# Optimization experiments

Measured on AMD Instinct MI355X. Metric: run time of the kernel, lower is better.

## Reference

```python
import jax, jax.numpy as jnp
import numpy as np

B, N = 16384, 4096
PERCENT_ON = 0.1
TEMPERATURE = 10.0  # training-mode temperature
K = int(round(N * PERCENT_ON))  # 410


def setup_inputs() -> dict:
    key = jax.random.key(0)
    k1, k2 = jax.random.split(key)
    x = jax.random.normal(k1, (B, N), dtype=jnp.float32)
    # Gumbel noise for sampling-without-replacement (Gumbel-top-k trick),
    # equivalent to torch.multinomial(softmax(x/T), k, replacement=False).
    gumbel = jax.random.gumbel(k2, (B, N), dtype=jnp.float32)
    return {"x": x, "gumbel": gumbel}


def reference(x, gumbel):
    # logits with temperature
    logits = x / TEMPERATURE
    # entropy of the categorical distribution per row, averaged (single stable pass)
    logp = jax.nn.log_softmax(logits, axis=-1)
    entropy = jnp.mean(-jnp.sum(jnp.exp(logp) * logp, axis=-1))
    # sample K winners without replacement via Gumbel-top-k
    _, idx = jax.lax.top_k(logits + gumbel, K)  # idx: [B, K]
    rows = jnp.arange(x.shape[0])[:, None]       # [B, 1]
    mask = jnp.zeros_like(x).at[rows, idx].set(1.0)
    out = x * mask  # relu=False path
    return out, entropy
```

## Files before the change

### kernel.cpp

```cpp
#include <hip/hip_runtime.h>
#include <math.h>

#define TPB 256
#define EPT 16
#define NN  4096
#define KSEL 410
#define CAP 1024

typedef float floatx4 __attribute__((ext_vector_type(4)));

__device__ __forceinline__ unsigned sortkey(float f) {
    unsigned u = __float_as_uint(f);
    unsigned m = (unsigned)(((int)u) >> 31);
    return u ^ (m | 0x80000000u);
}

template <bool USE_WS>
__global__ __launch_bounds__(TPB)
void skw_main(const float* __restrict__ x, const float* __restrict__ g,
              float* __restrict__ out, float* __restrict__ rowH,
              float* __restrict__ entAcc, float invB)
{
    const int row  = blockIdx.x;
    const int t    = threadIdx.x;
    const int w    = t >> 6;
    const int lane = t & 63;
    const size_t rbase = (size_t)row * NN;

    float    xv[EPT];
    unsigned key[EPT];
    unsigned bp[EPT / 4];

    __shared__ unsigned hist0[256][9];
    __shared__ unsigned wtot[4];
    __shared__ unsigned wtA[4], wtB[4];
    __shared__ float    fred[8];
    __shared__ unsigned sh_digit, sh_above, sh_cnt, sh_thr, sh_take;

    unsigned* list = &hist0[0][0];

    const float4* xp = reinterpret_cast<const float4*>(x + rbase);
    const float4* gp = reinterpret_cast<const float4*>(g + rbase);
    floatx4*      op = reinterpret_cast<floatx4*>(out + rbase);

    float sZ = 0.f, sZL = 0.f;
#pragma unroll
    for (int q = 0; q < EPT / 4; ++q) {
        float4 xx = xp[(q << 8) + t];
        float4 gg = gp[(q << 8) + t];
        float xa[4] = {xx.x, xx.y, xx.z, xx.w};
        float ga[4] = {gg.x, gg.y, gg.z, gg.w};
        unsigned pk = 0;
#pragma unroll
        for (int jj = 0; jj < 4; ++jj) {
            float xs = xa[jj];
            xv[4 * q + jj] = xs;
            float l = xs * 0.1f;
            float e = __expf(l);
            sZ  += e;
            sZL = __builtin_fmaf(e, l, sZL);
            float q10 = __builtin_fmaf(__builtin_fmaf(-10.0f, l, xs), 0.1f, l);
            float s = q10 + ga[jj];
            key[4 * q + jj] = sortkey(s);
            int b = (int)__builtin_fmaf(s, 16.0f, 64.0f);
            b = min(max(b, 0), 255);
            pk |= (unsigned)b << (8 * jj);
        }
        bp[q] = pk;
    }

#pragma unroll
    for (int sft = 32; sft >= 1; sft >>= 1) { sZ += __shfl_xor(sZ, sft); sZL += __shfl_xor(sZL, sft); }
    if (lane == 0) { fred[w] = sZ; fred[4 + w] = sZL; }

    unsigned* h0 = &hist0[0][0];
#pragma unroll
    for (int i = 0; i < 9; ++i) h0[t + 256 * i] = 0;
    if (t == 0) sh_cnt = 0;
    __syncthreads();

    if (t == 0) {
        float Z = fred[0] + fred[1] + fred[2] + fred[3];
        float L = fred[4] + fred[5] + fred[6] + fred[7];
        float H = __logf(Z) - L / Z;
        if (USE_WS) rowH[row] = H;
        else atomicAdd(entAcc, H * invB);
    }

#pragma unroll
    for (int q = 0; q < EPT / 4; ++q) {
        unsigned pk = bp[q];
#pragma unroll
        for (int jj = 0; jj < 4; ++jj)
            atomicAdd(&hist0[(pk >> (8 * jj)) & 255u][lane & 7], 1u);
    }
    __syncthreads();

    unsigned v = 0;
#pragma unroll
    for (int k = 0; k < 8; ++k) v += hist0[t][k];
#pragma unroll
    for (int sft = 1; sft < 64; sft <<= 1) {
        unsigned tmp = __shfl(v, lane + sft);
        v += (lane + sft < 64) ? tmp : 0u;
    }
    if (lane == 0) wtot[w] = v;
    unsigned vnext = __shfl(v, lane + 1);
    __syncthreads();
    unsigned Kr = KSEL;
    {
        unsigned hi = 0;
#pragma unroll
        for (int c = 0; c < 4; ++c) hi += (c > w) ? wtot[c] : 0u;
        unsigned cum     = v + hi;
        unsigned cumNext = ((lane < 63) ? vnext : 0u) + hi;
        if (cum >= Kr && cumNext < Kr) { sh_digit = (unsigned)t; sh_above = cumNext; }
    }
    __syncthreads();
    const unsigned Bstar = sh_digit;
    Kr -= sh_above;

    unsigned cm = 0;
#pragma unroll
    for (int q = 0; q < EPT / 4; ++q) {
        unsigned pk = bp[q];
#pragma unroll
        for (int jj = 0; jj < 4; ++jj)
            cm |= (((pk >> (8 * jj)) & 255u) == Bstar) ? (1u << (4 * q + jj)) : 0u;
    }
#pragma unroll
    for (int j = 0; j < EPT; ++j) {
        if ((cm >> j) & 1u) {
            unsigned p = atomicAdd(&sh_cnt, 1u);
            if (p < CAP) list[p] = key[j];
        }
    }
    __syncthreads();

    const unsigned M = sh_cnt;
    for (unsigned i = t; i < M; i += TPB) {
        unsigned ki = list[i];
        unsigned gt = 0, eqc = 0;
        for (unsigned j2 = 0; j2 < M; ++j2) {
            unsigned kj = list[j2];
            gt  += (kj > ki) ? 1u : 0u;
            eqc += (kj == ki) ? 1u : 0u;
        }
        if (gt < Kr && Kr <= gt + eqc) { sh_thr = ki; sh_take = Kr - gt; }
    }
    __syncthreads();
    const unsigned thr    = sh_thr;
    const unsigned KrTake = sh_take;

    unsigned eq[4];
#pragma unroll
    for (int q = 0; q < 4; ++q) {
        unsigned e = 0;
#pragma unroll
        for (int jj = 0; jj < 4; ++jj) e += (key[4 * q + jj] == thr) ? 1u : 0u;
        eq[q] = e;
    }
    unsigned wA = eq[0] | (eq[1] << 16);
    unsigned wB = eq[2] | (eq[3] << 16);
    unsigned sA = wA, sB = wB;
#pragma unroll
    for (int sft = 1; sft < 64; sft <<= 1) {
        unsigned ta = __shfl(sA, lane - sft);
        unsigned tb = __shfl(sB, lane - sft);
        if (lane >= sft) { sA += ta; sB += tb; }
    }
    if (lane == 63) { wtA[w] = sA; wtB[w] = sB; }
    __syncthreads();
    unsigned offA = 0, offB = 0, totA = 0, totB = 0;
#pragma unroll
    for (int c = 0; c < 4; ++c) {
        totA += wtA[c]; totB += wtB[c];
        if (c < w) { offA += wtA[c]; offB += wtB[c]; }
    }
    unsigned exA = offA + sA - wA;
    unsigned exB = offB + sB - wB;
    unsigned tot0 = totA & 0xFFFFu, tot1 = totA >> 16, tot2 = totB & 0xFFFFu;
    unsigned baseq[4] = {0u, tot0, tot0 + tot1, tot0 + tot1 + tot2};
    unsigned exq[4]   = {exA & 0xFFFFu, exA >> 16, exB & 0xFFFFu, exB >> 16};

#pragma unroll
    for (int q = 0; q < EPT / 4; ++q) {
        unsigned pos = baseq[q] + exq[q];
        float vals[4];
#pragma unroll
        for (int jj = 0; jj < 4; ++jj) {
            int j = 4 * q + jj;
            bool sel;
            if (key[j] > thr)       sel = true;
            else if (key[j] == thr) { sel = (pos < KrTake); ++pos; }
            else                    sel = false;
            vals[jj] = sel ? xv[j] : 0.0f;
        }
        floatx4 o4;
        o4.x = vals[0]; o4.y = vals[1]; o4.z = vals[2]; o4.w = vals[3];
        __builtin_nontemporal_store(o4, &op[(q << 8) + t]);
    }
}

__global__ void skw_zero(float* p) { *p = 0.0f; }

__global__ void skw_reduce(const float* __restrict__ rowH, float* __restrict__ outp, int B)
{
    __shared__ float red[256];
    int t = threadIdx.x;
    float s = 0.f;
    for (int i = t; i < B; i += 256) s += rowH[i];
    red[t] = s; __syncthreads();
    for (int st = 128; st > 0; st >>= 1) { if (t < st) red[t] += red[t + st]; __syncthreads(); }
    if (t == 0) *outp = red[0] / (float)B;
}

extern "C" void kernel_launch(void* const* d_in, const int* in_sizes, int n_in,
                              void* d_out, int out_size, void* d_ws, size_t ws_size,
                              hipStream_t stream)
{
    const float* x = (const float*)d_in[0];
    const float* g = (const float*)d_in[1];
    float* out = (float*)d_out;
    const int BN = in_sizes[0];
    const int B  = BN / NN;
    float* entp = out + (size_t)BN;

    if (ws_size >= (size_t)B * sizeof(float)) {
        float* rowH = (float*)d_ws;
        skw_main<true><<<B, TPB, 0, stream>>>(x, g, out, rowH, nullptr, 0.f);
        skw_reduce<<<1, 256, 0, stream>>>(rowH, entp, B);
    } else {
        skw_zero<<<1, 1, 0, stream>>>(entp);
        skw_main<false><<<B, TPB, 0, stream>>>(x, g, out, nullptr, entp, 1.0f / (float)B);
    }
}
```

Before: 166.9 us.

## Use 1024 threads per row with one float4 per thread

Each row block now has 1024 threads, and each thread handles a single float4 of x and gumbel instead of four. This drops the per-thread arrays and the packed 16-bit two-lane prefix scan, and uses 16 waves for the reductions and the tie-break scan. Histogram scanning stays on the first 4 waves, and both branches still hit the barrier. The aim is lower register pressure and more loads in flight on a kernel limited by memory bandwidth. The cost is more barrier participants and a longer cross-wave reduction.

```diff
diff --git a/kernel.cpp b/kernel.cpp
--- a/kernel.cpp
+++ b/kernel.cpp
@@ -1,8 +1,9 @@
 #include <hip/hip_runtime.h>
 #include <math.h>
 
-#define TPB 256
-#define EPT 16
+#define TPB 1024
+#define EPT 4
+#define NW  16
 #define NN  4096
 #define KSEL 410
 #define CAP 1024
@@ -27,14 +28,12 @@
     const int lane = t & 63;
     const size_t rbase = (size_t)row * NN;
 
-    float    xv[EPT];
     unsigned key[EPT];
-    unsigned bp[EPT / 4];
 
     __shared__ unsigned hist0[256][9];
     __shared__ unsigned wtot[4];
-    __shared__ unsigned wtA[4], wtB[4];
-    __shared__ float    fred[8];
+    __shared__ unsigned wt16[NW];
+    __shared__ float    fred[2 * NW];
     __shared__ unsigned sh_digit, sh_above, sh_cnt, sh_thr, sh_take;
 
     unsigned* list = &hist0[0][0];
@@ -43,96 +42,81 @@
     const float4* gp = reinterpret_cast<const float4*>(g + rbase);
     floatx4*      op = reinterpret_cast<floatx4*>(out + rbase);
 
+    float4 xx = xp[t];
+    float4 gg = gp[t];
+
+    float xa[4] = {xx.x, xx.y, xx.z, xx.w};
+    float ga[4] = {gg.x, gg.y, gg.z, gg.w};
     float sZ = 0.f, sZL = 0.f;
-#pragma unroll
-    for (int q = 0; q < EPT / 4; ++q) {
-        float4 xx = xp[(q << 8) + t];
-        float4 gg = gp[(q << 8) + t];
-        float xa[4] = {xx.x, xx.y, xx.z, xx.w};
-        float ga[4] = {gg.x, gg.y, gg.z, gg.w};
-        unsigned pk = 0;
-#pragma unroll
-        for (int jj = 0; jj < 4; ++jj) {
-            float xs = xa[jj];
-            xv[4 * q + jj] = xs;
-            float l = xs * 0.1f;
-            float e = __expf(l);
-            sZ  += e;
-            sZL = __builtin_fmaf(e, l, sZL);
-            float q10 = __builtin_fmaf(__builtin_fmaf(-10.0f, l, xs), 0.1f, l);
-            float s = q10 + ga[jj];
-            key[4 * q + jj] = sortkey(s);
-            int b = (int)__builtin_fmaf(s, 16.0f, 64.0f);
-            b = min(max(b, 0), 255);
-            pk |= (unsigned)b << (8 * jj);
-        }
-        bp[q] = pk;
+    unsigned pk = 0;
+#pragma unroll
+    for (int jj = 0; jj < 4; ++jj) {
+        float xs = xa[jj];
+        float l = xs * 0.1f;
+        float e = __expf(l);
+        sZ  += e;
+        sZL = __builtin_fmaf(e, l, sZL);
+        float q10 = __builtin_fmaf(__builtin_fmaf(-10.0f, l, xs), 0.1f, l);
+        float s = q10 + ga[jj];
+        key[jj] = sortkey(s);
+        int b = (int)__builtin_fmaf(s, 16.0f, 64.0f);
+        b = min(max(b, 0), 255);
+        pk |= (unsigned)b << (8 * jj);
     }
 
 #pragma unroll
     for (int sft = 32; sft >= 1; sft >>= 1) { sZ += __shfl_xor(sZ, sft); sZL += __shfl_xor(sZL, sft); }
-    if (lane == 0) { fred[w] = sZ; fred[4 + w] = sZL; }
+    if (lane == 0) { fred[w] = sZ; fred[NW + w] = sZL; }
 
     unsigned* h0 = &hist0[0][0];
-#pragma unroll
-    for (int i = 0; i < 9; ++i) h0[t + 256 * i] = 0;
+    for (int i = t; i < 256 * 9; i += TPB) h0[i] = 0;
     if (t == 0) sh_cnt = 0;
     __syncthreads();
 
     if (t == 0) {
-        float Z = fred[0] + fred[1] + fred[2] + fred[3];
-        float L = fred[4] + fred[5] + fred[6] + fred[7];
+        float Z = 0.f, L = 0.f;
+#pragma unroll
+        for (int c = 0; c < NW; ++c) { Z += fred[c]; L += fred[NW + c]; }
         float H = __logf(Z) - L / Z;
         if (USE_WS) rowH[row] = H;
         else atomicAdd(entAcc, H * invB);
     }
 
 #pragma unroll
-    for (int q = 0; q < EPT / 4; ++q) {
-        unsigned pk = bp[q];
-#pragma unroll
-        for (int jj = 0; jj < 4; ++jj)
-            atomicAdd(&hist0[(pk >> (8 * jj)) & 255u][lane & 7], 1u);
-    }
-    __syncthreads();
-
-    unsigned v = 0;
-#pragma unroll
-    for (int k = 0; k < 8; ++k) v += hist0[t][k];
-#pragma unroll
-    for (int sft = 1; sft < 64; sft <<= 1) {
-        unsigned tmp = __shfl(v, lane + sft);
-        v += (lane + sft < 64) ? tmp : 0u;
-    }
-    if (lane == 0) wtot[w] = v;
-    unsigned vnext = __shfl(v, lane + 1);
-    __syncthreads();
-    unsigned Kr = KSEL;
-    {
+    for (int jj = 0; jj < 4; ++jj)
+        atomicAdd(&hist0[(pk >> (8 * jj)) & 255u][lane & 7], 1u);
+    __syncthreads();
+
+    if (t < 256) {
+        unsigned v = 0;
+#pragma unroll
+        for (int k = 0; k < 8; ++k) v += hist0[t][k];
+#pragma unroll
+        for (int sft = 1; sft < 64; sft <<= 1) {
+            unsigned tmp = __shfl(v, lane + sft);
+            v += (lane + sft < 64) ? tmp : 0u;
+        }
+        if (lane == 0) wtot[w] = v;
+        unsigned vnext = __shfl(v, lane + 1);
+        __syncthreads();
         unsigned hi = 0;
 #pragma unroll
         for (int c = 0; c < 4; ++c) hi += (c > w) ? wtot[c] : 0u;
         unsigned cum     = v + hi;
         unsigned cumNext = ((lane < 63) ? vnext : 0u) + hi;
-        if (cum >= Kr && cumNext < Kr) { sh_digit = (unsigned)t; sh_above = cumNext; }
+        if (cum >= KSEL && cumNext < KSEL) { sh_digit = (unsigned)t; sh_above = cumNext; }
+    } else {
+        __syncthreads();
     }
     __syncthreads();
     const unsigned Bstar = sh_digit;
-    Kr -= sh_above;
-
-    unsigned cm = 0;
-#pragma unroll
-    for (int q = 0; q < EPT / 4; ++q) {
-        unsigned pk = bp[q];
-#pragma unroll
-        for (int jj = 0; jj < 4; ++jj)
-            cm |= (((pk >> (8 * jj)) & 255u) == Bstar) ? (1u << (4 * q + jj)) : 0u;
-    }
-#pragma unroll
-    for (int j = 0; j < EPT; ++j) {
-        if ((cm >> j) & 1u) {
+    const unsigned Kr = KSEL - sh_above;
+
+#pragma unroll
+    for (int jj = 0; jj < 4; ++jj) {
+        if (((pk >> (8 * jj)) & 255u) == Bstar) {
             unsigned p = atomicAdd(&sh_cnt, 1u);
-            if (p < CAP) list[p] = key[j];
+            if (p < CAP) list[p] = key[jj];
         }
     }
     __syncthreads();
@@ -152,54 +136,34 @@
     const unsigned thr    = sh_thr;
     const unsigned KrTake = sh_take;
 
-    unsigned eq[4];
-#pragma unroll
-    for (int q = 0; q < 4; ++q) {
-        unsigned e = 0;
-#pragma unroll
-        for (int jj = 0; jj < 4; ++jj) e += (key[4 * q + jj] == thr) ? 1u : 0u;
-        eq[q] = e;
-    }
-    unsigned wA = eq[0] | (eq[1] << 16);
-    unsigned wB = eq[2] | (eq[3] << 16);
-    unsigned sA = wA, sB = wB;
+    unsigned eq = 0;
+#pragma unroll
+    for (int jj = 0; jj < 4; ++jj) eq += (key[jj] == thr) ? 1u : 0u;
+    unsigned sv = eq;
 #pragma unroll
     for (int sft = 1; sft < 64; sft <<= 1) {
-        unsigned ta = __shfl(sA, lane - sft);
-        unsigned tb = __shfl(sB, lane - sft);
-        if (lane >= sft) { sA += ta; sB += tb; }
-    }
-    if (lane == 63) { wtA[w] = sA; wtB[w] = sB; }
-    __syncthreads();
-    unsigned offA = 0, offB = 0, totA = 0, totB = 0;
-#pragma unroll
-    for (int c = 0; c < 4; ++c) {
-        totA += wtA[c]; totB += wtB[c];
-        if (c < w) { offA += wtA[c]; offB += wtB[c]; }
-    }
-    unsigned exA = offA + sA - wA;
-    unsigned exB = offB + sB - wB;
-    unsigned tot0 = totA & 0xFFFFu, tot1 = totA >> 16, tot2 = totB & 0xFFFFu;
-    unsigned baseq[4] = {0u, tot0, tot0 + tot1, tot0 + tot1 + tot2};
-    unsigned exq[4]   = {exA & 0xFFFFu, exA >> 16, exB & 0xFFFFu, exB >> 16};
-
-#pragma unroll
-    for (int q = 0; q < EPT / 4; ++q) {
-        unsigned pos = baseq[q] + exq[q];
-        float vals[4];
-#pragma unroll
-        for (int jj = 0; jj < 4; ++jj) {
-            int j = 4 * q + jj;
-            bool sel;
-            if (key[j] > thr)       sel = true;
-            else if (key[j] == thr) { sel = (pos < KrTake); ++pos; }
-            else                    sel = false;
-            vals[jj] = sel ? xv[j] : 0.0f;
-        }
-        floatx4 o4;
-        o4.x = vals[0]; o4.y = vals[1]; o4.z = vals[2]; o4.w = vals[3];
-        __builtin_nontemporal_store(o4, &op[(q << 8) + t]);
-    }
+        unsigned tmp = __shfl(sv, lane - sft);
+        sv += (lane >= sft) ? tmp : 0u;
+    }
+    if (lane == 63) wt16[w] = sv;
+    __syncthreads();
+    unsigned offset = 0;
+#pragma unroll
+    for (int c = 0; c < NW; ++c) offset += (c < w) ? wt16[c] : 0u;
+    unsigned pos = offset + sv - eq;
+
+    float vals[4];
+#pragma unroll
+    for (int jj = 0; jj < 4; ++jj) {
+        bool sel;
+        if (key[jj] > thr)       sel = true;
+        else if (key[jj] == thr) { sel = (pos < KrTake); ++pos; }
+        else                     sel = false;
+        vals[jj] = sel ? xa[jj] : 0.0f;
+    }
+    floatx4 o4;
+    o4.x = vals[0]; o4.y = vals[1]; o4.z = vals[2]; o4.w = vals[3];
+    __builtin_nontemporal_store(o4, &op[t]);
 }
 
 __global__ void skw_zero(float* p) { *p = 0.0f; }
```

Measured after the change: 227.2 us. 36.2% more time.

## Process eight rows per block with double-buffered async global-to-LDS prefetch

Applied to the files above, without the earlier changes.

Each block now handles eight consecutive rows instead of one. While the current row is processed from LDS, the x and gumbel data for the next row are loaded into a second LDS buffer with global_load_lds, so load latency overlaps the histogram and selection work. The intent is to hide HBM latency and cut per-block launch overhead. The cost is a 64 KB LDS staging buffer per block, which lowers how many blocks can be resident per CU. The hand-written vmcnt waits also depend on how the earlier non-temporal stores are counted, and a wrong count could let a row be read before its prefetch has landed.

```diff
diff --git a/kernel.cpp b/kernel.cpp
--- a/kernel.cpp
+++ b/kernel.cpp
@@ -6,6 +6,7 @@
 #define NN  4096
 #define KSEL 410
 #define CAP 1024
+#define ROWS 8
 
 typedef float floatx4 __attribute__((ext_vector_type(4)));
 
@@ -15,22 +16,45 @@
     return u ^ (m | 0x80000000u);
 }
 
+__device__ __forceinline__ void dma16(const float* gsrc, float* lds) {
+    __builtin_amdgcn_global_load_lds(
+        (__attribute__((address_space(1))) void*)(void*)gsrc,
+        (__attribute__((address_space(3))) void*)(void*)lds,
+        16, 0, 0);
+}
+
+__device__ __forceinline__ void barsync() {
+    asm volatile("s_waitcnt lgkmcnt(0)" ::: "memory");
+    __builtin_amdgcn_s_barrier();
+}
+
+#define VMWAIT(N) do { \
+    asm volatile("s_waitcnt vmcnt(" #N ")" ::: "memory"); \
+    __builtin_amdgcn_sched_barrier(0); \
+} while (0)
+
+#define ISSUE_DMA(rw, b) do { \
+    const float* xr_ = x + (size_t)(rw) * NN; \
+    const float* gr_ = g + (size_t)(rw) * NN; \
+    float* sb_ = &stage[b][w * 2048]; \
+    _Pragma("unroll") \
+    for (int q_ = 0; q_ < 4; ++q_) { \
+        dma16(xr_ + q_ * 1024 + w * 256 + lane * 4, sb_ + q_ * 256); \
+        dma16(gr_ + q_ * 1024 + w * 256 + lane * 4, sb_ + 1024 + q_ * 256); \
+    } \
+} while (0)
+
 template <bool USE_WS>
 __global__ __launch_bounds__(TPB)
 void skw_main(const float* __restrict__ x, const float* __restrict__ g,
               float* __restrict__ out, float* __restrict__ rowH,
-              float* __restrict__ entAcc, float invB)
+              float* __restrict__ entAcc, float invB, int nrows)
 {
-    const int row  = blockIdx.x;
     const int t    = threadIdx.x;
     const int w    = t >> 6;
     const int lane = t & 63;
-    const size_t rbase = (size_t)row * NN;
-
-    float    xv[EPT];
-    unsigned key[EPT];
-    unsigned bp[EPT / 4];
-
+
+    __shared__ float    stage[2][8192];
     __shared__ unsigned hist0[256][9];
     __shared__ unsigned wtot[4];
     __shared__ unsigned wtA[4], wtB[4];
@@ -39,166 +63,183 @@
 
     unsigned* list = &hist0[0][0];
 
-    const float4* xp = reinterpret_cast<const float4*>(x + rbase);
-    const float4* gp = reinterpret_cast<const float4*>(g + rbase);
-    floatx4*      op = reinterpret_cast<floatx4*>(out + rbase);
-
-    float sZ = 0.f, sZL = 0.f;
-#pragma unroll
-    for (int q = 0; q < EPT / 4; ++q) {
-        float4 xx = xp[(q << 8) + t];
-        float4 gg = gp[(q << 8) + t];
-        float xa[4] = {xx.x, xx.y, xx.z, xx.w};
-        float ga[4] = {gg.x, gg.y, gg.z, gg.w};
-        unsigned pk = 0;
-#pragma unroll
-        for (int jj = 0; jj < 4; ++jj) {
-            float xs = xa[jj];
-            xv[4 * q + jj] = xs;
-            float l = xs * 0.1f;
-            float e = __expf(l);
-            sZ  += e;
-            sZL = __builtin_fmaf(e, l, sZL);
-            float q10 = __builtin_fmaf(__builtin_fmaf(-10.0f, l, xs), 0.1f, l);
-            float s = q10 + ga[jj];
-            key[4 * q + jj] = sortkey(s);
-            int b = (int)__builtin_fmaf(s, 16.0f, 64.0f);
-            b = min(max(b, 0), 255);
-            pk |= (unsigned)b << (8 * jj);
-        }
-        bp[q] = pk;
-    }
-
-#pragma unroll
-    for (int sft = 32; sft >= 1; sft >>= 1) { sZ += __shfl_xor(sZ, sft); sZL += __shfl_xor(sZL, sft); }
-    if (lane == 0) { fred[w] = sZ; fred[4 + w] = sZL; }
-
-    unsigned* h0 = &hist0[0][0];
-#pragma unroll
-    for (int i = 0; i < 9; ++i) h0[t + 256 * i] = 0;
-    if (t == 0) sh_cnt = 0;
-    __syncthreads();
-
-    if (t == 0) {
-        float Z = fred[0] + fred[1] + fred[2] + fred[3];
-        float L = fred[4] + fred[5] + fred[6] + fred[7];
-        float H = __logf(Z) - L / Z;
-        if (USE_WS) rowH[row] = H;
-        else atomicAdd(entAcc, H * invB);
-    }
-
-#pragma unroll
-    for (int q = 0; q < EPT / 4; ++q) {
-        unsigned pk = bp[q];
-#pragma unroll
-        for (int jj = 0; jj < 4; ++jj)
-            atomicAdd(&hist0[(pk >> (8 * jj)) & 255u][lane & 7], 1u);
-    }
-    __syncthreads();
-
-    unsigned v = 0;
-#pragma unroll
-    for (int k = 0; k < 8; ++k) v += hist0[t][k];
-#pragma unroll
-    for (int sft = 1; sft < 64; sft <<= 1) {
-        unsigned tmp = __shfl(v, lane + sft);
-        v += (lane + sft < 64) ? tmp : 0u;
-    }
-    if (lane == 0) wtot[w] = v;
-    unsigned vnext = __shfl(v, lane + 1);
-    __syncthreads();
-    unsigned Kr = KSEL;
-    {
-        unsigned hi = 0;
-#pragma unroll
-        for (int c = 0; c < 4; ++c) hi += (c > w) ? wtot[c] : 0u;
-        unsigned cum     = v + hi;
-        unsigned cumNext = ((lane < 63) ? vnext : 0u) + hi;
-        if (cum >= Kr && cumNext < Kr) { sh_digit = (unsigned)t; sh_above = cumNext; }
-    }
-    __syncthreads();
-    const unsigned Bstar = sh_digit;
-    Kr -= sh_above;
-
-    unsigned cm = 0;
-#pragma unroll
-    for (int q = 0; q < EPT / 4; ++q) {
-        unsigned pk = bp[q];
-#pragma unroll
-        for (int jj = 0; jj < 4; ++jj)
-            cm |= (((pk >> (8 * jj)) & 255u) == Bstar) ? (1u << (4 * q + jj)) : 0u;
-    }
-#pragma unroll
-    for (int j = 0; j < EPT; ++j) {
-        if ((cm >> j) & 1u) {
-            unsigned p = atomicAdd(&sh_cnt, 1u);
-            if (p < CAP) list[p] = key[j];
-        }
-    }
-    __syncthreads();
-
-    const unsigned M = sh_cnt;
-    for (unsigned i = t; i < M; i += TPB) {
-        unsigned ki = list[i];
-        unsigned gt = 0, eqc = 0;
-        for (unsigned j2 = 0; j2 < M; ++j2) {
-            unsigned kj = list[j2];
-            gt  += (kj > ki) ? 1u : 0u;
-            eqc += (kj == ki) ? 1u : 0u;
-        }
-        if (gt < Kr && Kr <= gt + eqc) { sh_thr = ki; sh_take = Kr - gt; }
-    }
-    __syncthreads();
-    const unsigned thr    = sh_thr;
-    const unsigned KrTake = sh_take;
-
-    unsigned eq[4];
-#pragma unroll
-    for (int q = 0; q < 4; ++q) {
-        unsigned e = 0;
-#pragma unroll
-        for (int jj = 0; jj < 4; ++jj) e += (key[4 * q + jj] == thr) ? 1u : 0u;
-        eq[q] = e;
-    }
-    unsigned wA = eq[0] | (eq[1] << 16);
-    unsigned wB = eq[2] | (eq[3] << 16);
-    unsigned sA = wA, sB = wB;
-#pragma unroll
-    for (int sft = 1; sft < 64; sft <<= 1) {
-        unsigned ta = __shfl(sA, lane - sft);
-        unsigned tb = __shfl(sB, lane - sft);
-        if (lane >= sft) { sA += ta; sB += tb; }
-    }
-    if (lane == 63) { wtA[w] = sA; wtB[w] = sB; }
-    __syncthreads();
-    unsigned offA = 0, offB = 0, totA = 0, totB = 0;
-#pragma unroll
-    for (int c = 0; c < 4; ++c) {
-        totA += wtA[c]; totB += wtB[c];
-        if (c < w) { offA += wtA[c]; offB += wtB[c]; }
-    }
-    unsigned exA = offA + sA - wA;
-    unsigned exB = offB + sB - wB;
-    unsigned tot0 = totA & 0xFFFFu, tot1 = totA >> 16, tot2 = totB & 0xFFFFu;
-    unsigned baseq[4] = {0u, tot0, tot0 + tot1, tot0 + tot1 + tot2};
-    unsigned exq[4]   = {exA & 0xFFFFu, exA >> 16, exB & 0xFFFFu, exB >> 16};
-
-#pragma unroll
-    for (int q = 0; q < EPT / 4; ++q) {
-        unsigned pos = baseq[q] + exq[q];
-        float vals[4];
-#pragma unroll
-        for (int jj = 0; jj < 4; ++jj) {
-            int j = 4 * q + jj;
-            bool sel;
-            if (key[j] > thr)       sel = true;
-            else if (key[j] == thr) { sel = (pos < KrTake); ++pos; }
-            else                    sel = false;
-            vals[jj] = sel ? xv[j] : 0.0f;
-        }
-        floatx4 o4;
-        o4.x = vals[0]; o4.y = vals[1]; o4.z = vals[2]; o4.w = vals[3];
-        __builtin_nontemporal_store(o4, &op[(q << 8) + t]);
+    const int r0 = blockIdx.x * ROWS;
+    if (r0 >= nrows) return;
+    const int rend = (r0 + ROWS < nrows) ? (r0 + ROWS) : nrows;
+
+    int cur = 0;
+    ISSUE_DMA(r0, 0);
+
+#pragma unroll 1
+    for (int row = r0; row < rend; ++row) {
+        if (row == r0) { VMWAIT(0); } else { VMWAIT(8); }
+
+        if (row + 1 < rend) ISSUE_DMA(row + 1, cur ^ 1);
+
+        const float4* sx = reinterpret_cast<const float4*>(&stage[cur][w * 2048]);
+
+        float    xc[EPT];
+        unsigned key[EPT];
+        unsigned bp[EPT / 4];
+        float sZ = 0.f, sZL = 0.f;
+#pragma unroll
+        for (int q = 0; q < EPT / 4; ++q) {
+            float4 xx = sx[q * 64 + lane];
+            float4 gg = sx[256 + q * 64 + lane];
+            float xa[4] = {xx.x, xx.y, xx.z, xx.w};
+            float ga[4] = {gg.x, gg.y, gg.z, gg.w};
+            unsigned pk = 0;
+#pragma unroll
+            for (int jj = 0; jj < 4; ++jj) {
+                float xs = xa[jj];
+                xc[4 * q + jj] = xs;
+                float l = xs * 0.1f;
+                float e = __expf(l);
+                sZ  += e;
+                sZL = __builtin_fmaf(e, l, sZL);
+                float q10 = __builtin_fmaf(__builtin_fmaf(-10.0f, l, xs), 0.1f, l);
+                float s = q10 + ga[jj];
+                key[4 * q + jj] = sortkey(s);
+                int b = (int)__builtin_fmaf(s, 16.0f, 64.0f);
+                b = min(max(b, 0), 255);
+                pk |= (unsigned)b << (8 * jj);
+            }
+            bp[q] = pk;
+        }
+
+#pragma unroll
+        for (int sft = 32; sft >= 1; sft >>= 1) { sZ += __shfl_xor(sZ, sft); sZL += __shfl_xor(sZL, sft); }
+        if (lane == 0) { fred[w] = sZ; fred[4 + w] = sZL; }
+
+        unsigned* h0 = &hist0[0][0];
+#pragma unroll
+        for (int i = 0; i < 9; ++i) h0[t + 256 * i] = 0;
+        if (t == 0) sh_cnt = 0;
+        barsync();
+
+        if (t == 0) {
+            float Z = fred[0] + fred[1] + fred[2] + fred[3];
+            float L = fred[4] + fred[5] + fred[6] + fred[7];
+            float H = __logf(Z) - L / Z;
+            if (USE_WS) rowH[row] = H;
+            else atomicAdd(entAcc, H * invB);
+        }
+
+#pragma unroll
+        for (int q = 0; q < EPT / 4; ++q) {
+            unsigned pk = bp[q];
+#pragma unroll
+            for (int jj = 0; jj < 4; ++jj)
+                atomicAdd(&hist0[(pk >> (8 * jj)) & 255u][lane & 7], 1u);
+        }
+        barsync();
+
+        unsigned v = 0;
+#pragma unroll
+        for (int k = 0; k < 8; ++k) v += hist0[t][k];
+#pragma unroll
+        for (int sft = 1; sft < 64; sft <<= 1) {
+            unsigned tmp = __shfl(v, lane + sft);
+            v += (lane + sft < 64) ? tmp : 0u;
+        }
+        if (lane == 0) wtot[w] = v;
+        unsigned vnext = __shfl(v, lane + 1);
+        barsync();
+        unsigned Kr = KSEL;
+        {
+            unsigned hi = 0;
+#pragma unroll
+            for (int c = 0; c < 4; ++c) hi += (c > w) ? wtot[c] : 0u;
+            unsigned cum     = v + hi;
+            unsigned cumNext = ((lane < 63) ? vnext : 0u) + hi;
+            if (cum >= Kr && cumNext < Kr) { sh_digit = (unsigned)t; sh_above = cumNext; }
+        }
+        barsync();
+        const unsigned Bstar = sh_digit;
+        Kr -= sh_above;
+
+        unsigned cm = 0;
+#pragma unroll
+        for (int q = 0; q < EPT / 4; ++q) {
+            unsigned pk = bp[q];
+#pragma unroll
+            for (int jj = 0; jj < 4; ++jj)
+                cm |= (((pk >> (8 * jj)) & 255u) == Bstar) ? (1u << (4 * q + jj)) : 0u;
+        }
+#pragma unroll
+        for (int j = 0; j < EPT; ++j) {
+            if ((cm >> j) & 1u) {
+                unsigned p = atomicAdd(&sh_cnt, 1u);
+                if (p < CAP) list[p] = key[j];
+            }
+        }
+        barsync();
+
+        const unsigned M = sh_cnt;
+        for (unsigned i = t; i < M; i += TPB) {
+            unsigned ki = list[i];
+            unsigned gt = 0, eqc = 0;
+            for (unsigned j2 = 0; j2 < M; ++j2) {
+                unsigned kj = list[j2];
+                gt  += (kj > ki) ? 1u : 0u;
+                eqc += (kj == ki) ? 1u : 0u;
+            }
+            if (gt < Kr && Kr <= gt + eqc) { sh_thr = ki; sh_take = Kr - gt; }
+        }
+        barsync();
+        const unsigned thr    = sh_thr;
+        const unsigned KrTake = sh_take;
+
+        unsigned eq[4];
+#pragma unroll
+        for (int q = 0; q < 4; ++q) {
+            unsigned e = 0;
+#pragma unroll
+            for (int jj = 0; jj < 4; ++jj) e += (key[4 * q + jj] == thr) ? 1u : 0u;
+            eq[q] = e;
+        }
+        unsigned wA = eq[0] | (eq[1] << 16);
+        unsigned wB = eq[2] | (eq[3] << 16);
+        unsigned sA = wA, sB = wB;
+#pragma unroll
+        for (int sft = 1; sft < 64; sft <<= 1) {
+            unsigned ta = __shfl(sA, lane - sft);
+            unsigned tb = __shfl(sB, lane - sft);
+            if (lane >= sft) { sA += ta; sB += tb; }
+        }
+        if (lane == 63) { wtA[w] = sA; wtB[w] = sB; }
+        barsync();
+        unsigned offA = 0, offB = 0, totA = 0, totB = 0;
+#pragma unroll
+        for (int c = 0; c < 4; ++c) {
+            totA += wtA[c]; totB += wtB[c];
+            if (c < w) { offA += wtA[c]; offB += wtB[c]; }
+        }
+        unsigned exA = offA + sA - wA;
+        unsigned exB = offB + sB - wB;
+        unsigned tot0 = totA & 0xFFFFu, tot1 = totA >> 16, tot2 = totB & 0xFFFFu;
+        unsigned baseq[4] = {0u, tot0, tot0 + tot1, tot0 + tot1 + tot2};
+        unsigned exq[4]   = {exA & 0xFFFFu, exA >> 16, exB & 0xFFFFu, exB >> 16};
+
+        floatx4* op = reinterpret_cast<floatx4*>(out + (size_t)row * NN);
+#pragma unroll
+        for (int q = 0; q < EPT / 4; ++q) {
+            unsigned pos = baseq[q] + exq[q];
+            float vals[4];
+#pragma unroll
+            for (int jj = 0; jj < 4; ++jj) {
+                int j = 4 * q + jj;
+                bool sel;
+                if (key[j] > thr)       sel = true;
+                else if (key[j] == thr) { sel = (pos < KrTake); ++pos; }
+                else                    sel = false;
+                vals[jj] = sel ? xc[j] : 0.0f;
+            }
+            floatx4 o4;
+            o4.x = vals[0]; o4.y = vals[1]; o4.z = vals[2]; o4.w = vals[3];
+            __builtin_nontemporal_store(o4, &op[(q << 8) + t]);
+        }
+        cur ^= 1;
     }
 }
 
@@ -225,13 +266,14 @@
     const int BN = in_sizes[0];
     const int B  = BN / NN;
     float* entp = out + (size_t)BN;
+    const int grid = (B + ROWS - 1) / ROWS;
 
     if (ws_size >= (size_t)B * sizeof(float)) {
         float* rowH = (float*)d_ws;
-        skw_main<true><<<B, TPB, 0, stream>>>(x, g, out, rowH, nullptr, 0.f);
+        skw_main<true><<<grid, TPB, 0, stream>>>(x, g, out, rowH, nullptr, 0.f, B);
         skw_reduce<<<1, 256, 0, stream>>>(rowH, entp, B);
     } else {
         skw_zero<<<1, 1, 0, stream>>>(entp);
-        skw_main<false><<<B, TPB, 0, stream>>>(x, g, out, nullptr, entp, 1.0f / (float)B);
+        skw_main<false><<<grid, TPB, 0, stream>>>(x, g, out, nullptr, entp, 1.0f / (float)B, B);
     }
 }
```

Result: slower. 238.7 us (+43.1%).
